# Kernel tuning notes

Measured on AMD Instinct MI355X. Metric: run time of the kernel, lower is better.

Reference implementation:

```python
import jax, jax.numpy as jnp
import numpy as np

N_NODES = 100000
IN_DIM, HID_DIM, OUT_DIM = 1433, 16, 7
N_EDGES = 3200000


def gcn_conv(x, edge_index, W, b, num_nodes):
    # add self loops
    loop = jnp.arange(num_nodes, dtype=edge_index.dtype)
    src = jnp.concatenate([edge_index[0], loop])  # [E+N]
    dst = jnp.concatenate([edge_index[1], loop])
    h = x @ W + b  # [N, out]
    # degree computed on row (edge_index[0]) as in the torch code
    deg = jax.ops.segment_sum(jnp.ones_like(src, dtype=h.dtype), src,
                              num_segments=num_nodes)
    dis = deg ** -0.5  # self-loops guarantee deg >= 1
    norm = dis[src] * dis[dst]  # [E+N]
    msg = norm[:, None] * h[src]  # gather + scale
    return jax.ops.segment_sum(msg, dst, num_segments=num_nodes)  # scatter-add


def setup_inputs() -> dict:
    key = jax.random.key(0)
    k1, k2, k3, k4, k5, k6 = jax.random.split(key, 6)
    x = jax.random.normal(k1, (N_NODES, IN_DIM), dtype=jnp.float32)
    edge_index = jax.random.randint(k2, (2, N_EDGES), 0, N_NODES, dtype=jnp.int64)
    s1 = 1.0 / np.sqrt(IN_DIM)
    s2 = 1.0 / np.sqrt(HID_DIM)
    W1 = jax.random.uniform(k3, (IN_DIM, HID_DIM), jnp.float32, -s1, s1)
    b1 = jax.random.uniform(k4, (HID_DIM,), jnp.float32, -s1, s1)
    W2 = jax.random.uniform(k5, (HID_DIM, OUT_DIM), jnp.float32, -s2, s2)
    b2 = jax.random.uniform(k6, (OUT_DIM,), jnp.float32, -s2, s2)
    return {"x": x, "edge_index": edge_index, "W1": W1, "b1": b1,
            "W2": W2, "b2": b2}


def reference(x, edge_index, W1, b1, W2, b2):
    n = x.shape[0]
    h = gcn_conv(x, edge_index, W1, b1, n)
    h = jax.nn.relu(h)
    # dropout is inactive in eval mode (training=False)
    h = gcn_conv(h, edge_index, W2, b2, n)
    return jax.nn.log_softmax(h, axis=1)
```

## Files before the change

kernel.cpp:

```cpp
#include <hip/hip_runtime.h>
#include <math.h>

constexpr int IN_DIM = 1433;
constexpr int HID    = 16;
constexpr int OUTD   = 7;

__device__ __forceinline__ int edge_get(const int* __restrict__ ei, long long idx, int is64) {
    return is64 ? ei[2 * idx] : ei[idx];
}

__global__ void k_detect(const int* __restrict__ ei, int* __restrict__ flag) {
    __shared__ int nzsh;
    if (threadIdx.x == 0) nzsh = 0;
    __syncthreads();
    int nz = 0;
    for (int i = threadIdx.x; i < 2048; i += blockDim.x)
        nz |= (ei[2 * i + 1] != 0) ? 1 : 0;
    if (nz) nzsh = 1;
    __syncthreads();
    if (threadIdx.x == 0) *flag = (nzsh == 0) ? 1 : 0;
}

__global__ void k_init_new(int* __restrict__ deg, int* __restrict__ cnt, int n) {
    int i = blockIdx.x * blockDim.x + threadIdx.x;
    if (i < n) { deg[i] = 1; cnt[i] = 0; }
}

__global__ void k_deg_finish(float* __restrict__ dis, int n) {
    int i = blockIdx.x * blockDim.x + threadIdx.x;
    if (i < n) {
        int v = ((const int*)dis)[i];
        dis[i] = rsqrtf((float)v);
    }
}

__global__ void k_hist2(const int* __restrict__ ei, int E, const int* __restrict__ flag,
                        int* __restrict__ deg, int* __restrict__ cnt,
                        int* __restrict__ packed) {
    int e = blockIdx.x * blockDim.x + threadIdx.x;
    if (e >= E) return;
    int is64 = *flag;
    int s = edge_get(ei, e, is64);
    int d = edge_get(ei, (long long)E + e, is64);
    atomicAdd(&deg[s], 1);
    int slot = atomicAdd(&cnt[d], 1);
    packed[e] = (d << 14) | (slot & 16383);
}

__global__ void k_place(const int* __restrict__ ei, int E, const int* __restrict__ flag,
                        const int* __restrict__ packed, const int* __restrict__ rp,
                        int* __restrict__ csr) {
    int e = blockIdx.x * blockDim.x + threadIdx.x;
    if (e >= E) return;
    int is64 = *flag;
    int s  = edge_get(ei, e, is64);
    int p  = packed[e];
    int d  = p >> 14;
    int sl = p & 16383;
    csr[rp[d] + sl] = s;
}

__global__ __launch_bounds__(256) void k_scan1(const int* __restrict__ cnt,
                                               int* __restrict__ bsum, int n) {
    __shared__ int sh[256];
    int t = threadIdx.x;
    int base = blockIdx.x * 1024 + t * 4;
    int s = 0;
    #pragma unroll
    for (int j = 0; j < 4; ++j) {
        int i = base + j;
        if (i < n) s += cnt[i];
    }
    sh[t] = s; __syncthreads();
    for (int o = 128; o > 0; o >>= 1) {
        if (t < o) sh[t] += sh[t + o];
        __syncthreads();
    }
    if (t == 0) bsum[blockIdx.x] = sh[0];
}

__global__ __launch_bounds__(256) void k_scan2(const int* __restrict__ bsum,
                                               int* __restrict__ boff,
                                               int* __restrict__ rp,
                                               int nb, int n, int E) {
    __shared__ int sh[256];
    int t = threadIdx.x;
    int v = (t < nb) ? bsum[t] : 0;
    sh[t] = v; __syncthreads();
    for (int o = 1; o < 256; o <<= 1) {
        int tmp = (t >= o) ? sh[t - o] : 0;
        __syncthreads();
        sh[t] += tmp;
        __syncthreads();
    }
    boff[t] = sh[t] - v;
    if (t == 0) rp[n] = E;
}

__global__ __launch_bounds__(256) void k_scan3(const int* __restrict__ cnt,
                                               const int* __restrict__ boff,
                                               int* __restrict__ rp, int n) {
    __shared__ int sh[256];
    int t = threadIdx.x;
    int base = blockIdx.x * 1024 + t * 4;
    int c[4];
    int s = 0;
    #pragma unroll
    for (int j = 0; j < 4; ++j) {
        int i = base + j;
        c[j] = (i < n) ? cnt[i] : 0;
        s += c[j];
    }
    sh[t] = s; __syncthreads();
    for (int o = 1; o < 256; o <<= 1) {
        int tmp = (t >= o) ? sh[t - o] : 0;
        __syncthreads();
        sh[t] += tmp;
        __syncthreads();
    }
    int run = boff[blockIdx.x] + sh[t] - s;
    #pragma unroll
    for (int j = 0; j < 4; ++j) {
        int i = base + j;
        if (i < n) rp[i] = run;
        run += c[j];
    }
}

__global__ __launch_bounds__(128) void k_gemm1(
        const float* __restrict__ x, const float* __restrict__ W1,
        const float* __restrict__ b1, float* __restrict__ h1, int n) {
    constexpr int BK = 32, XST = 36;
    __shared__ __align__(16) float xs[128 * XST];
    __shared__ __align__(16) float wsm[BK * HID];
    const int t    = threadIdx.x;
    const int c4   = t & 3;
    const int rq   = t >> 2;
    const int row0 = blockIdx.x * 128;

    float xreg[32];
    float wreg[4];
    float4 acc[4];
    #pragma unroll
    for (int j = 0; j < 4; ++j) acc[j] = make_float4(0.f, 0.f, 0.f, 0.f);

    auto issue = [&](int kt) {
        #pragma unroll
        for (int i = 0; i < 32; ++i) {
            int idx  = t + 128 * i;
            int srow = idx >> 5;
            int scol = idx & 31;
            int gr   = row0 + srow;
            int col  = kt + scol;
            float v = 0.f;
            if (gr < n && col < IN_DIM) v = x[(long long)gr * IN_DIM + col];
            xreg[i] = v;
        }
        #pragma unroll
        for (int u = 0; u < 4; ++u) {
            int idx = t + 128 * u;
            int kk  = idx >> 4;
            wreg[u] = (kt + kk < IN_DIM) ? W1[(kt + kk) * HID + (idx & 15)] : 0.f;
        }
    };
    auto commit = [&]() {
        #pragma unroll
        for (int i = 0; i < 32; ++i) {
            int idx  = t + 128 * i;
            int srow = idx >> 5;
            int scol = idx & 31;
            xs[srow * XST + scol] = xreg[i];
        }
        #pragma unroll
        for (int u = 0; u < 4; ++u) wsm[t + 128 * u] = wreg[u];
    };

    const int nkt = (IN_DIM + BK - 1) / BK;
    issue(0);
    for (int it = 0; it < nkt; ++it) {
        commit();
        __syncthreads();
        if (it + 1 < nkt) issue((it + 1) * BK);
        #pragma unroll
        for (int k4 = 0; k4 < BK / 4; ++k4) {
            int k = k4 * 4;
            float4 w0 = *(const float4*)&wsm[(k + 0) * HID + c4 * 4];
            float4 w1 = *(const float4*)&wsm[(k + 1) * HID + c4 * 4];
            float4 w2 = *(const float4*)&wsm[(k + 2) * HID + c4 * 4];
            float4 w3 = *(const float4*)&wsm[(k + 3) * HID + c4 * 4];
            #pragma unroll
            for (int j = 0; j < 4; ++j) {
                float4 xv = *(const float4*)&xs[(rq + 32 * j) * XST + k];
                acc[j].x += xv.x * w0.x + xv.y * w1.x + xv.z * w2.x + xv.w * w3.x;
                acc[j].y += xv.x * w0.y + xv.y * w1.y + xv.z * w2.y + xv.w * w3.y;
                acc[j].z += xv.x * w0.z + xv.y * w1.z + xv.z * w2.z + xv.w * w3.z;
                acc[j].w += xv.x * w0.w + xv.y * w1.w + xv.z * w2.w + xv.w * w3.w;
            }
        }
        __syncthreads();
    }

    float4 bv = *(const float4*)&b1[c4 * 4];
    #pragma unroll
    for (int j = 0; j < 4; ++j) {
        int gr = row0 + rq + 32 * j;
        if (gr < n) {
            float4 hv;
            hv.x = acc[j].x + bv.x;
            hv.y = acc[j].y + bv.y;
            hv.z = acc[j].z + bv.z;
            hv.w = acc[j].w + bv.w;
            *(float4*)&h1[(long long)gr * HID + c4 * 4] = hv;
        }
    }
}

__global__ void k_scale(const float* __restrict__ dis, const float* __restrict__ in,
                        float* __restrict__ out, int n, int squared) {
    int i = blockIdx.x * blockDim.x + threadIdx.x;
    if (i >= n * 4) return;
    int row = i >> 2;
    float d = dis[row];
    if (squared) d *= d;
    float4 v = *(const float4*)&in[(long long)i * 4];
    v.x *= d; v.y *= d; v.z *= d; v.w *= d;
    *(float4*)&out[(long long)i * 4] = v;
}

__global__ __launch_bounds__(256) void k_gather1f(
        const int* __restrict__ rp, const int* __restrict__ csr,
        const float* __restrict__ dis, const float* __restrict__ hs1,
        const float* __restrict__ W2, const float* __restrict__ b2,
        float* __restrict__ hs2, int n) {
    __shared__ float w2s[HID * OUTD];
    __shared__ float b2s[OUTD];
    int t = threadIdx.x;
    if (t < HID * OUTD) w2s[t] = W2[t];
    if (t < OUTD) b2s[t] = b2[t];
    __syncthreads();

    int tid  = blockIdx.x * blockDim.x + t;
    int node = tid >> 2;
    int q    = tid & 3;
    if (node >= n) return;

    float4 acc = *(const float4*)&hs1[(long long)node * HID + q * 4];

    int i = rp[node], end = rp[node + 1];
    for (; i + 4 <= end; i += 4) {
        int s0 = csr[i], s1 = csr[i + 1], s2 = csr[i + 2], s3 = csr[i + 3];
        float4 h0 = *(const float4*)&hs1[(long long)s0 * HID + q * 4];
        float4 h1 = *(const float4*)&hs1[(long long)s1 * HID + q * 4];
        float4 h2 = *(const float4*)&hs1[(long long)s2 * HID + q * 4];
        float4 h3 = *(const float4*)&hs1[(long long)s3 * HID + q * 4];
        acc.x += (h0.x + h1.x) + (h2.x + h3.x);
        acc.y += (h0.y + h1.y) + (h2.y + h3.y);
        acc.z += (h0.z + h1.z) + (h2.z + h3.z);
        acc.w += (h0.w + h1.w) + (h2.w + h3.w);
    }
    for (; i < end; ++i) {
        int s = csr[i];
        float4 h = *(const float4*)&hs1[(long long)s * HID + q * 4];
        acc.x += h.x; acc.y += h.y; acc.z += h.z; acc.w += h.w;
    }

    float dn = dis[node];
    float r0 = fmaxf(dn * acc.x, 0.f), r1 = fmaxf(dn * acc.y, 0.f);
    float r2 = fmaxf(dn * acc.z, 0.f), r3 = fmaxf(dn * acc.w, 0.f);
    float p[OUTD];
    #pragma unroll
    for (int j = 0; j < OUTD; ++j) {
        p[j] = r0 * w2s[(q * 4 + 0) * OUTD + j]
             + r1 * w2s[(q * 4 + 1) * OUTD + j]
             + r2 * w2s[(q * 4 + 2) * OUTD + j]
             + r3 * w2s[(q * 4 + 3) * OUTD + j];
    }
    #pragma unroll
    for (int j = 0; j < OUTD; ++j) {
        p[j] += __shfl_xor(p[j], 1, 4);
        p[j] += __shfl_xor(p[j], 2, 4);
    }
    hs2[(long long)node * OUTD + q] = dn * (p[q] + b2s[q]);
    if (q < 3) hs2[(long long)node * OUTD + q + 4] = dn * (p[q + 4] + b2s[q + 4]);
}

__global__ __launch_bounds__(256) void k_gather2(
        const int* __restrict__ rp, const int* __restrict__ csr,
        const float* __restrict__ dis, const float* __restrict__ hs2,
        float* __restrict__ out, int n) {
    int t = threadIdx.x;
    int node = blockIdx.x * 32 + (t >> 3);
    int q = t & 7;
    if (node >= n) return;
    float acc = -1e30f;
    if (q < OUTD) {
        acc = hs2[(long long)node * OUTD + q];
        int i = rp[node], end = rp[node + 1];
        for (; i + 8 <= end; i += 8) {
            int s0 = csr[i],     s1 = csr[i + 1], s2 = csr[i + 2], s3 = csr[i + 3];
            int s4 = csr[i + 4], s5 = csr[i + 5], s6 = csr[i + 6], s7 = csr[i + 7];
            float v0 = hs2[(long long)s0 * OUTD + q];
            float v1 = hs2[(long long)s1 * OUTD + q];
            float v2 = hs2[(long long)s2 * OUTD + q];
            float v3 = hs2[(long long)s3 * OUTD + q];
            float v4 = hs2[(long long)s4 * OUTD + q];
            float v5 = hs2[(long long)s5 * OUTD + q];
            float v6 = hs2[(long long)s6 * OUTD + q];
            float v7 = hs2[(long long)s7 * OUTD + q];
            acc += ((v0 + v1) + (v2 + v3)) + ((v4 + v5) + (v6 + v7));
        }
        for (; i < end; ++i) {
            int s = csr[i];
            acc += hs2[(long long)s * OUTD + q];
        }
        acc *= dis[node];
    }
    float m = acc;
    #pragma unroll
    for (int o = 1; o < 8; o <<= 1) m = fmaxf(m, __shfl_xor(m, o, 8));
    float ex = (q < OUTD) ? expf(acc - m) : 0.f;
    float ss = ex;
    #pragma unroll
    for (int o = 1; o < 8; o <<= 1) ss += __shfl_xor(ss, o, 8);
    if (q < OUTD) out[(long long)node * OUTD + q] = acc - m - logf(ss);
}

__global__ void k_deg_init(int* __restrict__ deg, int n) {
    int i = blockIdx.x * blockDim.x + threadIdx.x;
    if (i < n) deg[i] = 1;
}

__global__ void k_deg_count(const int* __restrict__ ei, int E,
                            const int* __restrict__ flag, int* __restrict__ deg) {
    int e = blockIdx.x * blockDim.x + threadIdx.x;
    if (e >= E) return;
    int is64 = *flag;
    int s = edge_get(ei, e, is64);
    atomicAdd(&deg[s], 1);
}

__global__ void k_agg1(const int* __restrict__ ei, int E, const int* __restrict__ flag,
                       const float* __restrict__ dis, const float* __restrict__ h1,
                       float* __restrict__ a1) {
    long long tid = (long long)blockIdx.x * blockDim.x + threadIdx.x;
    int e = (int)(tid >> 2);
    int q = (int)(tid & 3);
    if (e >= E) return;
    int is64 = *flag;
    int s = edge_get(ei, e, is64);
    int d = edge_get(ei, (long long)E + e, is64);
    float nrm = dis[s] * dis[d];
    float4 v = *(const float4*)&h1[(long long)s * HID + q * 4];
    float* o = &a1[(long long)d * HID + q * 4];
    atomicAdd(o + 0, nrm * v.x);
    atomicAdd(o + 1, nrm * v.y);
    atomicAdd(o + 2, nrm * v.z);
    atomicAdd(o + 3, nrm * v.w);
}

__global__ __launch_bounds__(256) void k_gemm2(
        const float* __restrict__ a1, const float* __restrict__ W2,
        const float* __restrict__ b2, const float* __restrict__ dis,
        float* __restrict__ h2, float* __restrict__ a2, int n) {
    __shared__ float w2s[HID * OUTD];
    __shared__ float b2s[OUTD];
    int t = threadIdx.x;
    if (t < HID * OUTD) w2s[t] = W2[t];
    if (t < OUTD) b2s[t] = b2[t];
    __syncthreads();
    int r = blockIdx.x * blockDim.x + t;
    if (r >= n) return;
    float a[16];
    #pragma unroll
    for (int i = 0; i < 4; ++i) {
        float4 v = *(const float4*)&a1[(long long)r * HID + i * 4];
        a[4 * i + 0] = fmaxf(v.x, 0.f);
        a[4 * i + 1] = fmaxf(v.y, 0.f);
        a[4 * i + 2] = fmaxf(v.z, 0.f);
        a[4 * i + 3] = fmaxf(v.w, 0.f);
    }
    float dd = 0.f;
    if (a2) { float d = dis[r]; dd = d * d; }
    #pragma unroll
    for (int j = 0; j < OUTD; ++j) {
        float acc = b2s[j];
        #pragma unroll
        for (int k = 0; k < HID; ++k) acc += a[k] * w2s[k * OUTD + j];
        h2[(long long)r * OUTD + j] = acc;
        if (a2) a2[(long long)r * OUTD + j] = dd * acc;
    }
}

__global__ void k_agg2(const int* __restrict__ ei, int E, const int* __restrict__ flag,
                       const float* __restrict__ dis, const float* __restrict__ h2,
                       float* __restrict__ a2) {
    long long tid = (long long)blockIdx.x * blockDim.x + threadIdx.x;
    int e = (int)(tid >> 1);
    int q = (int)(tid & 1);
    if (e >= E) return;
    int is64 = *flag;
    int s = edge_get(ei, e, is64);
    int d = edge_get(ei, (long long)E + e, is64);
    float nrm = dis[s] * dis[d];
    int cnt = q ? 3 : 4;
    long long bs = (long long)s * OUTD + q * 4;
    long long bd = (long long)d * OUTD + q * 4;
    #pragma unroll
    for (int j = 0; j < 4; ++j)
        if (j < cnt) atomicAdd(&a2[bd + j], nrm * h2[bs + j]);
}

__global__ void k_lsm(const float* __restrict__ a2, float* __restrict__ out, int n) {
    int r = blockIdx.x * blockDim.x + threadIdx.x;
    if (r >= n) return;
    float v[OUTD];
    #pragma unroll
    for (int j = 0; j < OUTD; ++j) v[j] = a2[(long long)r * OUTD + j];
    float m = v[0];
    #pragma unroll
    for (int j = 1; j < OUTD; ++j) m = fmaxf(m, v[j]);
    float ssum = 0.f;
    #pragma unroll
    for (int j = 0; j < OUTD; ++j) ssum += expf(v[j] - m);
    float l = logf(ssum);
    #pragma unroll
    for (int j = 0; j < OUTD; ++j) out[(long long)r * OUTD + j] = v[j] - m - l;
}

extern "C" void kernel_launch(void* const* d_in, const int* in_sizes, int n_in,
                              void* d_out, int out_size, void* d_ws, size_t ws_size,
                              hipStream_t stream) {
    const float* x  = (const float*)d_in[0];
    const int*   ei = (const int*)d_in[1];
    const float* W1 = (const float*)d_in[2];
    const float* b1 = (const float*)d_in[3];
    const float* W2 = (const float*)d_in[4];
    const float* b2 = (const float*)d_in[5];
    float* out = (float*)d_out;

    const int N = in_sizes[0] / IN_DIM;
    const int E = in_sizes[1] / 2;

    const int TPB = 256;
    const int gN  = (N + TPB - 1) / TPB;
    const int gE  = (E + TPB - 1) / TPB;
    const int gG1 = (N + 127) / 128;
    const int NB  = (N + 1023) / 1024;

    float* ws = (float*)d_ws;
    size_t o = 0;
    auto take = [&](size_t cnt) { size_t r = o; o += (cnt + 127) & ~(size_t)127; return r; };

    size_t off_dis  = take((size_t)N);
    size_t off_flag = take(64);
    size_t off_cnt  = take((size_t)N);
    size_t off_rp   = take((size_t)N + 1);
    size_t off_bs   = take(256);
    size_t off_bo   = take(256);
    size_t off_pk   = take((size_t)E);
    size_t off_csr  = take((size_t)E);
    size_t off_h1   = take((size_t)N * HID);
    size_t off_h2   = take((size_t)N * OUTD);
    size_t need_new = o * sizeof(float);

    if (ws_size >= need_new) {
        float* dis  = ws + off_dis;
        int*   degi = (int*)dis;
        int*   flag = (int*)(ws + off_flag);
        int*   cnt  = (int*)(ws + off_cnt);
        int*   rp   = (int*)(ws + off_rp);
        int*   bs   = (int*)(ws + off_bs);
        int*   bo   = (int*)(ws + off_bo);
        int*   pk   = (int*)(ws + off_pk);
        int*   csr  = (int*)(ws + off_csr);
        float* h1   = ws + off_h1;
        float* hs2  = ws + off_h2;

        k_detect<<<1, 256, 0, stream>>>(ei, flag);
        k_init_new<<<gN, TPB, 0, stream>>>(degi, cnt, N);
        k_hist2<<<gE, TPB, 0, stream>>>(ei, E, flag, degi, cnt, pk);
        k_deg_finish<<<gN, TPB, 0, stream>>>(dis, N);
        k_scan1<<<NB, 256, 0, stream>>>(cnt, bs, N);
        k_scan2<<<1, 256, 0, stream>>>(bs, bo, rp, NB, N, E);
        k_scan3<<<NB, 256, 0, stream>>>(cnt, bo, rp, N);
        k_place<<<gE, TPB, 0, stream>>>(ei, E, flag, pk, rp, csr);
        k_gemm1<<<gG1, 128, 0, stream>>>(x, W1, b1, h1, N);
        k_scale<<<(int)(((long long)N * 4 + TPB - 1) / TPB), TPB, 0, stream>>>(
            dis, h1, h1, N, 0);
        k_gather1f<<<(int)(((long long)N * 4 + TPB - 1) / TPB), TPB, 0, stream>>>(
            rp, csr, dis, h1, W2, b2, hs2, N);
        k_gather2<<<(N + 31) / 32, 256, 0, stream>>>(rp, csr, dis, hs2, out, N);
    } else {
        o = 0;
        size_t f_dis  = take((size_t)N);
        size_t f_flag = take(64);
        size_t f_h1   = take((size_t)N * HID);
        size_t f_a1   = take((size_t)N * HID);
        size_t f_h2   = take((size_t)N * OUTD);
        size_t f_a2   = take((size_t)N * OUTD);

        float* dis  = ws + f_dis;
        int*   degi = (int*)dis;
        int*   flag = (int*)(ws + f_flag);
        float* h1   = ws + f_h1;
        float* a1   = ws + f_a1;
        float* h2   = ws + f_h2;
        float* a2   = ws + f_a2;

        int g4E = (int)(((long long)4 * E + TPB - 1) / TPB);
        int g2E = (int)(((long long)2 * E + TPB - 1) / TPB);

        k_detect<<<1, 256, 0, stream>>>(ei, flag);
        k_deg_init<<<gN, TPB, 0, stream>>>(degi, N);
        k_deg_count<<<gE, TPB, 0, stream>>>(ei, E, flag, degi);
        k_deg_finish<<<gN, TPB, 0, stream>>>(dis, N);
        k_gemm1<<<gG1, 128, 0, stream>>>(x, W1, b1, h1, N);
        k_scale<<<(int)(((long long)N * 4 + TPB - 1) / TPB), TPB, 0, stream>>>(
            dis, h1, a1, N, 1);
        k_agg1<<<g4E, TPB, 0, stream>>>(ei, E, flag, dis, h1, a1);
        k_gemm2<<<gN, TPB, 0, stream>>>(a1, W2, b2, dis, h2, a2, N);
        k_agg2<<<g2E, TPB, 0, stream>>>(ei, E, flag, dis, h2, a2);
        k_lsm<<<gN, TPB, 0, stream>>>(a2, out, N);
    }
}
```

Baseline: 633.1 us.

## Overlap edge histogram with first GEMM in one launch and fuse small kernels

Merges the edge histogram (degree and in-count atomics) into the first dense GEMM kernel as extra grid-stride blocks, so atomic-bound work runs alongside the bandwidth-bound read of x. It also folds format detection into the init kernel and the rsqrt degree finish into the first scan pass, removing several launches. The histogram blocks now use a fixed block count with a grid-stride loop, which may change atomic contention and block scheduling order.

```diff
diff --git a/kernel.cpp b/kernel.cpp
--- a/kernel.cpp
+++ b/kernel.cpp
@@ -9,134 +9,50 @@
     return is64 ? ei[2 * idx] : ei[idx];
 }
 
-__global__ void k_detect(const int* __restrict__ ei, int* __restrict__ flag) {
-    __shared__ int nzsh;
-    if (threadIdx.x == 0) nzsh = 0;
-    __syncthreads();
-    int nz = 0;
-    for (int i = threadIdx.x; i < 2048; i += blockDim.x)
-        nz |= (ei[2 * i + 1] != 0) ? 1 : 0;
-    if (nz) nzsh = 1;
-    __syncthreads();
-    if (threadIdx.x == 0) *flag = (nzsh == 0) ? 1 : 0;
-}
-
-__global__ void k_init_new(int* __restrict__ deg, int* __restrict__ cnt, int n) {
+__global__ void k_detect_init(const int* __restrict__ ei, int* __restrict__ flag,
+                              int* __restrict__ deg, int* __restrict__ cnt, int n) {
     int i = blockIdx.x * blockDim.x + threadIdx.x;
     if (i < n) { deg[i] = 1; cnt[i] = 0; }
-}
-
-__global__ void k_deg_finish(float* __restrict__ dis, int n) {
-    int i = blockIdx.x * blockDim.x + threadIdx.x;
-    if (i < n) {
-        int v = ((const int*)dis)[i];
-        dis[i] = rsqrtf((float)v);
-    }
-}
-
-__global__ void k_hist2(const int* __restrict__ ei, int E, const int* __restrict__ flag,
-                        int* __restrict__ deg, int* __restrict__ cnt,
-                        int* __restrict__ packed) {
-    int e = blockIdx.x * blockDim.x + threadIdx.x;
-    if (e >= E) return;
-    int is64 = *flag;
-    int s = edge_get(ei, e, is64);
-    int d = edge_get(ei, (long long)E + e, is64);
-    atomicAdd(&deg[s], 1);
-    int slot = atomicAdd(&cnt[d], 1);
-    packed[e] = (d << 14) | (slot & 16383);
-}
-
-__global__ void k_place(const int* __restrict__ ei, int E, const int* __restrict__ flag,
-                        const int* __restrict__ packed, const int* __restrict__ rp,
-                        int* __restrict__ csr) {
-    int e = blockIdx.x * blockDim.x + threadIdx.x;
-    if (e >= E) return;
-    int is64 = *flag;
-    int s  = edge_get(ei, e, is64);
-    int p  = packed[e];
-    int d  = p >> 14;
-    int sl = p & 16383;
-    csr[rp[d] + sl] = s;
-}
-
-__global__ __launch_bounds__(256) void k_scan1(const int* __restrict__ cnt,
-                                               int* __restrict__ bsum, int n) {
-    __shared__ int sh[256];
-    int t = threadIdx.x;
-    int base = blockIdx.x * 1024 + t * 4;
-    int s = 0;
-    #pragma unroll
-    for (int j = 0; j < 4; ++j) {
-        int i = base + j;
-        if (i < n) s += cnt[i];
-    }
-    sh[t] = s; __syncthreads();
-    for (int o = 128; o > 0; o >>= 1) {
-        if (t < o) sh[t] += sh[t + o];
-        __syncthreads();
-    }
-    if (t == 0) bsum[blockIdx.x] = sh[0];
-}
-
-__global__ __launch_bounds__(256) void k_scan2(const int* __restrict__ bsum,
-                                               int* __restrict__ boff,
-                                               int* __restrict__ rp,
-                                               int nb, int n, int E) {
-    __shared__ int sh[256];
-    int t = threadIdx.x;
-    int v = (t < nb) ? bsum[t] : 0;
-    sh[t] = v; __syncthreads();
-    for (int o = 1; o < 256; o <<= 1) {
-        int tmp = (t >= o) ? sh[t - o] : 0;
-        __syncthreads();
-        sh[t] += tmp;
-        __syncthreads();
-    }
-    boff[t] = sh[t] - v;
-    if (t == 0) rp[n] = E;
-}
-
-__global__ __launch_bounds__(256) void k_scan3(const int* __restrict__ cnt,
-                                               const int* __restrict__ boff,
-                                               int* __restrict__ rp, int n) {
-    __shared__ int sh[256];
-    int t = threadIdx.x;
-    int base = blockIdx.x * 1024 + t * 4;
-    int c[4];
-    int s = 0;
-    #pragma unroll
-    for (int j = 0; j < 4; ++j) {
-        int i = base + j;
-        c[j] = (i < n) ? cnt[i] : 0;
-        s += c[j];
-    }
-    sh[t] = s; __syncthreads();
-    for (int o = 1; o < 256; o <<= 1) {
-        int tmp = (t >= o) ? sh[t - o] : 0;
-        __syncthreads();
-        sh[t] += tmp;
-        __syncthreads();
-    }
-    int run = boff[blockIdx.x] + sh[t] - s;
-    #pragma unroll
-    for (int j = 0; j < 4; ++j) {
-        int i = base + j;
-        if (i < n) rp[i] = run;
-        run += c[j];
-    }
-}
-
-__global__ __launch_bounds__(128) void k_gemm1(
+    if (blockIdx.x == 0) {
+        __shared__ int nzsh;
+        if (threadIdx.x == 0) nzsh = 0;
+        __syncthreads();
+        int nz = 0;
+        for (int j = threadIdx.x; j < 2048; j += blockDim.x)
+            nz |= (ei[2 * j + 1] != 0) ? 1 : 0;
+        if (nz) nzsh = 1;
+        __syncthreads();
+        if (threadIdx.x == 0) *flag = (nzsh == 0) ? 1 : 0;
+    }
+}
+
+__global__ __launch_bounds__(128) void k_gemm1h(
         const float* __restrict__ x, const float* __restrict__ W1,
-        const float* __restrict__ b1, float* __restrict__ h1, int n) {
+        const float* __restrict__ b1, float* __restrict__ h1, int n,
+        const int* __restrict__ ei, int E, const int* __restrict__ flag,
+        int* __restrict__ deg, int* __restrict__ cnt, int* __restrict__ packed,
+        int nHist) {
+    if ((int)blockIdx.x < nHist) {
+        int is64 = *flag;
+        long long stride = (long long)nHist * blockDim.x;
+        for (long long e = (long long)blockIdx.x * blockDim.x + threadIdx.x;
+             e < E; e += stride) {
+            int s = edge_get(ei, e, is64);
+            int d = edge_get(ei, (long long)E + e, is64);
+            atomicAdd(&deg[s], 1);
+            int slot = atomicAdd(&cnt[d], 1);
+            packed[e] = (d << 14) | (slot & 16383);
+        }
+        return;
+    }
+
     constexpr int BK = 32, XST = 36;
     __shared__ __align__(16) float xs[128 * XST];
     __shared__ __align__(16) float wsm[BK * HID];
     const int t    = threadIdx.x;
     const int c4   = t & 3;
     const int rq   = t >> 2;
-    const int row0 = blockIdx.x * 128;
+    const int row0 = ((int)blockIdx.x - nHist) * 128;
 
     float xreg[32];
     float wreg[4];
@@ -213,6 +129,91 @@
             *(float4*)&h1[(long long)gr * HID + c4 * 4] = hv;
         }
     }
+}
+
+__global__ __launch_bounds__(256) void k_scan1(const int* __restrict__ cnt,
+                                               int* __restrict__ bsum,
+                                               float* __restrict__ dis, int n) {
+    __shared__ int sh[256];
+    int t = threadIdx.x;
+    int base = blockIdx.x * 1024 + t * 4;
+    int s = 0;
+    #pragma unroll
+    for (int j = 0; j < 4; ++j) {
+        int i = base + j;
+        if (i < n) {
+            s += cnt[i];
+            int v = ((const int*)dis)[i];
+            dis[i] = rsqrtf((float)v);
+        }
+    }
+    sh[t] = s; __syncthreads();
+    for (int o = 128; o > 0; o >>= 1) {
+        if (t < o) sh[t] += sh[t + o];
+        __syncthreads();
+    }
+    if (t == 0) bsum[blockIdx.x] = sh[0];
+}
+
+__global__ __launch_bounds__(256) void k_scan2(const int* __restrict__ bsum,
+                                               int* __restrict__ boff,
+                                               int* __restrict__ rp,
+                                               int nb, int n, int E) {
+    __shared__ int sh[256];
+    int t = threadIdx.x;
+    int v = (t < nb) ? bsum[t] : 0;
+    sh[t] = v; __syncthreads();
+    for (int o = 1; o < 256; o <<= 1) {
+        int tmp = (t >= o) ? sh[t - o] : 0;
+        __syncthreads();
+        sh[t] += tmp;
+        __syncthreads();
+    }
+    boff[t] = sh[t] - v;
+    if (t == 0) rp[n] = E;
+}
+
+__global__ __launch_bounds__(256) void k_scan3(const int* __restrict__ cnt,
+                                               const int* __restrict__ boff,
+                                               int* __restrict__ rp, int n) {
+    __shared__ int sh[256];
+    int t = threadIdx.x;
+    int base = blockIdx.x * 1024 + t * 4;
+    int c[4];
+    int s = 0;
+    #pragma unroll
+    for (int j = 0; j < 4; ++j) {
+        int i = base + j;
+        c[j] = (i < n) ? cnt[i] : 0;
+        s += c[j];
+    }
+    sh[t] = s; __syncthreads();
+    for (int o = 1; o < 256; o <<= 1) {
+        int tmp = (t >= o) ? sh[t - o] : 0;
+        __syncthreads();
+        sh[t] += tmp;
+        __syncthreads();
+    }
+    int run = boff[blockIdx.x] + sh[t] - s;
+    #pragma unroll
+    for (int j = 0; j < 4; ++j) {
+        int i = base + j;
+        if (i < n) rp[i] = run;
+        run += c[j];
+    }
+}
+
+__global__ void k_place(const int* __restrict__ ei, int E, const int* __restrict__ flag,
+                        const int* __restrict__ packed, const int* __restrict__ rp,
+                        int* __restrict__ csr) {
+    int e = blockIdx.x * blockDim.x + threadIdx.x;
+    if (e >= E) return;
+    int is64 = *flag;
+    int s  = edge_get(ei, e, is64);
+    int p  = packed[e];
+    int d  = p >> 14;
+    int sl = p & 16383;
+    csr[rp[d] + sl] = s;
 }
 
 __global__ void k_scale(const float* __restrict__ dis, const float* __restrict__ in,
@@ -325,6 +326,18 @@
     if (q < OUTD) out[(long long)node * OUTD + q] = acc - m - logf(ss);
 }
 
+__global__ void k_detect(const int* __restrict__ ei, int* __restrict__ flag) {
+    __shared__ int nzsh;
+    if (threadIdx.x == 0) nzsh = 0;
+    __syncthreads();
+    int nz = 0;
+    for (int i = threadIdx.x; i < 2048; i += blockDim.x)
+        nz |= (ei[2 * i + 1] != 0) ? 1 : 0;
+    if (nz) nzsh = 1;
+    __syncthreads();
+    if (threadIdx.x == 0) *flag = (nzsh == 0) ? 1 : 0;
+}
+
 __global__ void k_deg_init(int* __restrict__ deg, int n) {
     int i = blockIdx.x * blockDim.x + threadIdx.x;
     if (i < n) deg[i] = 1;
@@ -337,6 +350,14 @@
     int is64 = *flag;
     int s = edge_get(ei, e, is64);
     atomicAdd(&deg[s], 1);
+}
+
+__global__ void k_deg_finish(float* __restrict__ dis, int n) {
+    int i = blockIdx.x * blockDim.x + threadIdx.x;
+    if (i < n) {
+        int v = ((const int*)dis)[i];
+        dis[i] = rsqrtf((float)v);
+    }
 }
 
 __global__ void k_agg1(const int* __restrict__ ei, int E, const int* __restrict__ flag,
@@ -446,6 +467,7 @@
     const int gE  = (E + TPB - 1) / TPB;
     const int gG1 = (N + 127) / 128;
     const int NB  = (N + 1023) / 1024;
+    const int nHist = 512;
 
     float* ws = (float*)d_ws;
     size_t o = 0;
@@ -476,15 +498,13 @@
         float* h1   = ws + off_h1;
         float* hs2  = ws + off_h2;
 
-        k_detect<<<1, 256, 0, stream>>>(ei, flag);
-        k_init_new<<<gN, TPB, 0, stream>>>(degi, cnt, N);
-        k_hist2<<<gE, TPB, 0, stream>>>(ei, E, flag, degi, cnt, pk);
-        k_deg_finish<<<gN, TPB, 0, stream>>>(dis, N);
-        k_scan1<<<NB, 256, 0, stream>>>(cnt, bs, N);
+        k_detect_init<<<gN, TPB, 0, stream>>>(ei, flag, degi, cnt, N);
+        k_gemm1h<<<nHist + gG1, 128, 0, stream>>>(x, W1, b1, h1, N,
+                                                  ei, E, flag, degi, cnt, pk, nHist);
+        k_scan1<<<NB, 256, 0, stream>>>(cnt, bs, dis, N);
         k_scan2<<<1, 256, 0, stream>>>(bs, bo, rp, NB, N, E);
         k_scan3<<<NB, 256, 0, stream>>>(cnt, bo, rp, N);
         k_place<<<gE, TPB, 0, stream>>>(ei, E, flag, pk, rp, csr);
-        k_gemm1<<<gG1, 128, 0, stream>>>(x, W1, b1, h1, N);
         k_scale<<<(int)(((long long)N * 4 + TPB - 1) / TPB), TPB, 0, stream>>>(
             dis, h1, h1, N, 0);
         k_gather1f<<<(int)(((long long)N * 4 + TPB - 1) / TPB), TPB, 0, stream>>>(
@@ -514,7 +534,8 @@
         k_deg_init<<<gN, TPB, 0, stream>>>(degi, N);
         k_deg_count<<<gE, TPB, 0, stream>>>(ei, E, flag, degi);
         k_deg_finish<<<gN, TPB, 0, stream>>>(dis, N);
-        k_gemm1<<<gG1, 128, 0, stream>>>(x, W1, b1, h1, N);
+        k_gemm1h<<<gG1, 128, 0, stream>>>(x, W1, b1, h1, N,
+                                          ei, E, flag, nullptr, nullptr, nullptr, 0);
         k_scale<<<(int)(((long long)N * 4 + TPB - 1) / TPB), TPB, 0, stream>>>(
             dis, h1, a1, N, 1);
         k_agg1<<<g4E, TPB, 0, stream>>>(ei, E, flag, dis, h1, a1);
```

New measurement: 668.1 us. 5.5% more time.
